# Kernel optimization log

Measured on AMD Instinct MI355X. Metric: run time of the kernel, lower is better.

## Reference

```python
import jax, jax.numpy as jnp
import numpy as np

ROPE_THETA = 10000.0


def apply_rope(q, k, cos, sin):
    # q,k: [B,H,S,D]; cos,sin: [S,D/2] -> broadcast [1,1,S,D/2]
    def rot(t):
        t2 = t.reshape(*t.shape[:-1], -1, 2)  # [B,H,S,D/2,2]
        te, to = t2[..., 0], t2[..., 1]
        c = cos[None, None, :, :]
        s = sin[None, None, :, :]
        re = te * c - to * s
        im = te * s + to * c
        return jnp.stack([re, im], axis=-1).reshape(t.shape)
    return rot(q), rot(k)


def setup_inputs() -> dict:
    key = jax.random.key(0)
    ks = jax.random.split(key, 4)
    B, S, D, H = 2, 2048, 1024, 16
    hd = D // H
    x = jax.random.normal(ks[0], (B, S, D), dtype=jnp.float32)
    # causal boolean mask (True = keep)
    mask = jnp.tril(jnp.ones((S, S), dtype=bool))[None, None]
    # rotary tables
    inv_freq = 1.0 / (ROPE_THETA ** (jnp.arange(0, hd, 2, dtype=jnp.float32) / hd))  # [hd/2]
    t = jnp.arange(S, dtype=jnp.float32)
    ang = t[:, None] * inv_freq[None, :]  # [S, hd/2]
    freqs_cos = jnp.cos(ang)
    freqs_sin = jnp.sin(ang)
    W_qkv = jax.random.normal(ks[1], (D, 3 * D), dtype=jnp.float32) * 0.02
    b_qkv = jnp.zeros((3 * D,), dtype=jnp.float32)
    W_o = jax.random.normal(ks[2], (D, D), dtype=jnp.float32) * 0.02
    b_o = jnp.zeros((D,), dtype=jnp.float32)
    return {"x": x, "mask": mask, "freqs_cos": freqs_cos, "freqs_sin": freqs_sin,
            "W_qkv": W_qkv, "b_qkv": b_qkv, "W_o": W_o, "b_o": b_o}


def reference(x, mask, freqs_cos, freqs_sin, W_qkv, b_qkv, W_o, b_o):
    B, S, D = x.shape
    H = 16
    hd = D // H
    scale = hd ** -0.5
    qkv = x @ W_qkv + b_qkv  # [B,S,3D]
    q, k, v = jnp.split(qkv, 3, axis=-1)
    q = q.reshape(B, S, H, hd).transpose(0, 2, 1, 3)  # [B,H,S,hd]
    k = k.reshape(B, S, H, hd).transpose(0, 2, 1, 3)
    v = v.reshape(B, S, H, hd).transpose(0, 2, 1, 3)
    q, k = apply_rope(q, k, freqs_cos, freqs_sin)
    scores = jnp.einsum('bhqd,bhkd->bhqk', q, k) * scale
    scores = jnp.where(mask, scores, jnp.finfo(scores.dtype).min)
    attn = jax.nn.softmax(scores, axis=-1)
    out = jnp.einsum('bhqk,bhkd->bhqd', attn, v)
    out = out.transpose(0, 2, 1, 3).reshape(B, S, D)
    return out @ W_o + b_o
```

## Files before the change

kernel.cpp:

```cpp
#include <hip/hip_runtime.h>
#include <hip/hip_bf16.h>
#include <stdint.h>

typedef unsigned short u16;
typedef __attribute__((ext_vector_type(8))) __bf16 bf16x8;
typedef __attribute__((ext_vector_type(4))) float f32x4;
typedef __attribute__((ext_vector_type(16))) float f32x16;
typedef __attribute__((ext_vector_type(8))) u16 u16x8;

__device__ __forceinline__ u16 f2bf(float f) {
  union { float f; unsigned int u; } v; v.f = f;
  unsigned int r = v.u + 0x7fffu + ((v.u >> 16) & 1u);
  return (u16)(r >> 16);
}
__device__ __forceinline__ unsigned pack2(float lo, float hi) {
  return (unsigned)f2bf(lo) | ((unsigned)f2bf(hi) << 16);
}

__device__ __forceinline__ f32x4 mfma16(bf16x8 a, bf16x8 b, f32x4 c) {
  return __builtin_amdgcn_mfma_f32_16x16x32_bf16(a, b, c, 0, 0, 0);
}
__device__ __forceinline__ f32x16 mfma32(bf16x8 a, bf16x8 b, f32x16 c) {
  return __builtin_amdgcn_mfma_f32_32x32x16_bf16(a, b, c, 0, 0, 0);
}

__device__ __forceinline__ void gload16(const void* g, void* l) {
  __builtin_amdgcn_global_load_lds((const __attribute__((address_space(1))) void*)g,
                                   (__attribute__((address_space(3))) void*)l,
                                   16, 0, 0);
}

__global__ void cast_bf16_kernel(const float* __restrict__ in, u16* __restrict__ out, int n) {
  int i = (blockIdx.x * 256 + threadIdx.x) * 8;
  if (i >= n) return;
  const float4* p = (const float4*)(in + i);
  float4 a = p[0], b = p[1];
  u16x8 o;
  o[0] = f2bf(a.x); o[1] = f2bf(a.y); o[2] = f2bf(a.z); o[3] = f2bf(a.w);
  o[4] = f2bf(b.x); o[5] = f2bf(b.y); o[6] = f2bf(b.z); o[7] = f2bf(b.w);
  *(u16x8*)(out + i) = o;
}

__global__ void transpose_cast_k(const float* __restrict__ in, u16* __restrict__ out,
                                 int R, int Ccols) {
  __shared__ float tile[64][65];
  const int c0 = (int)blockIdx.x << 6, r0 = (int)blockIdx.y << 6;
  const int tx = threadIdx.x & 63, ty = threadIdx.x >> 6;
#pragma unroll
  for (int i = ty; i < 64; i += 4)
    tile[i][tx] = in[(size_t)(r0 + i) * Ccols + c0 + tx];
  __syncthreads();
#pragma unroll
  for (int i = ty; i < 64; i += 4)
    out[(size_t)(c0 + i) * R + r0 + tx] = f2bf(tile[tx][i]);
}

__global__ __launch_bounds__(256, 2)
void gemm_bt(const u16* __restrict__ A, const u16* __restrict__ Bt,
             const float* __restrict__ bias, float* __restrict__ C,
             int M, int N, int K) {
  __shared__ u16 As[128 * 32];
  __shared__ u16 Bs[128 * 32];
  const int nb = N >> 7;
  const int m0 = (int)(blockIdx.x / nb) << 7;
  const int n0 = (int)(blockIdx.x % nb) << 7;
  const int tid = threadIdx.x;
  const int l = tid & 63, lg = l >> 4, ll = l & 15;
  const int w = tid >> 6;
  const int wr = (w >> 1) << 6, wc = (w & 1) << 6;
  const int srow = tid >> 2, scol = (tid & 3) << 3;
  const u16* ga = A + (size_t)(m0 + srow) * K + scol;
  const u16* gb = Bt + (size_t)(n0 + srow) * K + scol;
  u16* la0 = &As[srow * 32 + scol];
  u16* la1 = &As[(srow + 64) * 32 + scol];
  u16* lb0 = &Bs[srow * 32 + scol];
  u16* lb1 = &Bs[(srow + 64) * 32 + scol];
  const size_t K64 = (size_t)64 * K;
  f32x4 acc[4][4] = {};
  for (int kt = 0; kt < K; kt += 32) {
    gload16(ga + kt, la0);
    gload16(ga + kt + K64, la1);
    gload16(gb + kt, lb0);
    gload16(gb + kt + K64, lb1);
    __syncthreads();
    bf16x8 a[4], b[4];
#pragma unroll
    for (int i = 0; i < 4; ++i) {
      a[i] = *(const bf16x8*)&As[(wr + i * 16 + ll) * 32 + lg * 8];
      b[i] = *(const bf16x8*)&Bs[(wc + i * 16 + ll) * 32 + lg * 8];
    }
#pragma unroll
    for (int mi = 0; mi < 4; ++mi)
#pragma unroll
      for (int ni = 0; ni < 4; ++ni)
        acc[mi][ni] = mfma16(a[mi], b[ni], acc[mi][ni]);
    __syncthreads();
  }
#pragma unroll
  for (int mi = 0; mi < 4; ++mi) {
#pragma unroll
    for (int r = 0; r < 4; ++r) {
      const int row = m0 + wr + mi * 16 + lg * 4 + r;
      float* crow = C + (size_t)row * N + n0 + wc;
#pragma unroll
      for (int ni = 0; ni < 4; ++ni)
        crow[ni * 16 + ll] = acc[mi][ni][r] + bias[n0 + wc + ni * 16 + ll];
    }
  }
}

__global__ void rope_split_k(const float* __restrict__ qkv,
                             const float* __restrict__ fc, const float* __restrict__ fs,
                             u16* __restrict__ qr, u16* __restrict__ kr) {
  const int t = blockIdx.x;
  const int b = t >> 11, s = t & 2047;
  const int h = threadIdx.x >> 5, i = threadIdx.x & 31;
  const float c = fc[s * 32 + i], sn = fs[s * 32 + i];
  const float* qp = qkv + (size_t)t * 3072 + (h << 6) + 2 * i;
  const float qe = qp[0], qo = qp[1];
  const float ke = qp[1024], ko = qp[1025];
  const size_t ob = (((size_t)((b << 4) + h) << 11) + s) * 64 + 2 * i;
  qr[ob]     = f2bf((qe * c - qo * sn) * 0.125f);
  qr[ob + 1] = f2bf((qe * sn + qo * c) * 0.125f);
  kr[ob]     = f2bf(ke * c - ko * sn);
  kr[ob + 1] = f2bf(ke * sn + ko * c);
}

__global__ void v_transpose_k(const float* __restrict__ qkv, u16* __restrict__ vt) {
  __shared__ float tile[64][65];
  const int bh = blockIdx.x;
  const int b = bh >> 4, h = bh & 15;
  const int s0 = (int)blockIdx.y << 6;
  const int tx = threadIdx.x & 63, ty = threadIdx.x >> 6;
#pragma unroll
  for (int i = ty; i < 64; i += 4)
    tile[i][tx] = qkv[(size_t)((b << 11) + s0 + i) * 3072 + 2048 + (h << 6) + tx];
  __syncthreads();
#pragma unroll
  for (int i = ty; i < 64; i += 4)
    vt[((size_t)(bh << 6) + i) * 2048 + s0 + tx] = f2bf(tile[tx][i]);
}

__global__ __launch_bounds__(256, 2)
void attn_k(const u16* __restrict__ qr, const u16* __restrict__ kr,
            const u16* __restrict__ vt, u16* __restrict__ aout) {
  __shared__ __align__(16) char kvlds[16384];
  const int bi = (int)blockIdx.x;
  const int bh = bi & 31;
  const int qt = (bi < 256) ? (15 - (bi >> 5)) : ((bi - 256) >> 5);
  const int tid = threadIdx.x;
  const int w = tid >> 6, l = tid & 63, hi = l >> 5, ql = l & 31;
  const u16* Q  = qr + (size_t)bh * (2048 * 64);
  const u16* Kp = kr + (size_t)bh * (2048 * 64);
  const u16* Vp = vt + (size_t)bh * (64 * 2048);
  const int q0w = (qt << 7) + (w << 5);
  const int qg = q0w + ql;
  bf16x8 qf[4];
#pragma unroll
  for (int mi = 0; mi < 4; ++mi)
    qf[mi] = *(const bf16x8*)&Q[(size_t)qg * 64 + mi * 16 + hi * 8];
  const int sr = tid >> 2, sc = (tid & 3) * 32;
  const int wo0 = (sr * 128 + sc) ^ ((sr & 7) << 4);
  const int wo1 = (sr * 128 + sc + 16) ^ ((sr & 7) << 4);
  const char* kga = (const char*)(Kp + (size_t)sr * 64) + sc;
  const char* vga = (const char*)(Vp + (size_t)sr * 2048) + sc;
  const int swz = (ql & 7) << 4;
  f32x16 oa = {}, ob = {};
  float mrow = -1e30f, lp = 0.f;
  const int nch = 2 * qt + 2;
  uint4 sk0 = *(const uint4*)(kga), sk1 = *(const uint4*)(kga + 16);
  uint4 sv0 = *(const uint4*)(vga), sv1 = *(const uint4*)(vga + 16);
  for (int ch = 0; ch < nch; ++ch) {
    asm volatile("s_waitcnt vmcnt(0)" ::: "memory");
    asm volatile("s_barrier" ::: "memory");
    *(uint4*)(kvlds + wo0) = sk0;
    *(uint4*)(kvlds + wo1) = sk1;
    *(uint4*)(kvlds + 8192 + wo0) = sv0;
    *(uint4*)(kvlds + 8192 + wo1) = sv1;
    if (ch + 1 < nch) {
      const size_t kof = (size_t)(ch + 1) * 8192;
      const size_t vof = (size_t)(ch + 1) * 128;
      sk0 = *(const uint4*)(kga + kof); sk1 = *(const uint4*)(kga + kof + 16);
      sv0 = *(const uint4*)(vga + vof); sv1 = *(const uint4*)(vga + vof + 16);
    }
    asm volatile("s_waitcnt lgkmcnt(0)" ::: "memory");
    asm volatile("s_barrier" ::: "memory");
    const int kb = ch << 6;
    if (kb > q0w + 31) continue;
    f32x16 s0 = {}, s1 = {};
#pragma unroll
    for (int mi = 0; mi < 4; ++mi) {
      const int cb = mi * 32 + hi * 16;
      const bf16x8 k0 = *(const bf16x8*)(kvlds + ((ql * 128 + cb) ^ swz));
      const bf16x8 k1 = *(const bf16x8*)(kvlds + (((32 + ql) * 128 + cb) ^ swz));
      s0 = mfma32(k0, qf[mi], s0);
      s1 = mfma32(k1, qf[mi], s1);
    }
    if (kb + 63 > q0w) {
#pragma unroll
      for (int r = 0; r < 16; ++r) {
        const int kvo = (r & 3) + 8 * (r >> 2) + 4 * hi;
        if (kb + kvo > qg) s0[r] = -1e30f;
        if (kb + 32 + kvo > qg) s1[r] = -1e30f;
      }
    }
    float mx = s0[0];
#pragma unroll
    for (int r = 1; r < 16; ++r) mx = fmaxf(mx, s0[r]);
#pragma unroll
    for (int r = 0; r < 16; ++r) mx = fmaxf(mx, s1[r]);
    mx = fmaxf(mx, __shfl_xor(mx, 32));
    if (!__all(mx <= mrow + 8.f)) {
      const float mn = fmaxf(mrow, mx);
      const float esc = __expf(mrow - mn);
      mrow = mn;
      lp *= esc;
#pragma unroll
      for (int r = 0; r < 16; ++r) { oa[r] *= esc; ob[r] *= esc; }
    }
    float p0[16], p1[16];
#pragma unroll
    for (int r = 0; r < 16; ++r) {
      p0[r] = __expf(s0[r] - mrow);
      p1[r] = __expf(s1[r] - mrow);
      lp += p0[r] + p1[r];
    }
    bf16x8 pb[4];
#pragma unroll
    for (int s = 0; s < 2; ++s) {
      const float* ps = s ? p1 : p0;
#pragma unroll
      for (int j = 0; j < 2; ++j) {
        const unsigned X0 = pack2(ps[j * 8 + 0], ps[j * 8 + 1]);
        const unsigned X1 = pack2(ps[j * 8 + 2], ps[j * 8 + 3]);
        const unsigned Y0 = pack2(ps[j * 8 + 4], ps[j * 8 + 5]);
        const unsigned Y1 = pack2(ps[j * 8 + 6], ps[j * 8 + 7]);
        const unsigned sX0 = (unsigned)__shfl_xor((int)X0, 32);
        const unsigned sX1 = (unsigned)__shfl_xor((int)X1, 32);
        const unsigned sY0 = (unsigned)__shfl_xor((int)Y0, 32);
        const unsigned sY1 = (unsigned)__shfl_xor((int)Y1, 32);
        union { unsigned u[4]; bf16x8 v; } t;
        t.u[0] = hi ? sY0 : X0;
        t.u[1] = hi ? sY1 : X1;
        t.u[2] = hi ? Y0 : sX0;
        t.u[3] = hi ? Y1 : sX1;
        pb[s * 2 + j] = t.v;
      }
    }
#pragma unroll
    for (int jj = 0; jj < 4; ++jj) {
      const int cb = jj * 32 + hi * 16;
      const bf16x8 va = *(const bf16x8*)(kvlds + 8192 + ((ql * 128 + cb) ^ swz));
      const bf16x8 vb = *(const bf16x8*)(kvlds + 8192 + (((32 + ql) * 128 + cb) ^ swz));
      oa = mfma32(va, pb[jj], oa);
      ob = mfma32(vb, pb[jj], ob);
    }
  }
  lp += __shfl_xor(lp, 32);
  const float inv = 1.0f / lp;
  const int hcol = (bh & 15) << 6;
  const int tok = ((bh >> 4) << 11) + qg;
  unsigned* orow = (unsigned*)(aout + (size_t)tok * 1024 + hcol);
#pragma unroll
  for (int r = 0; r < 16; r += 2) {
    const int d0 = (r & 3) + 8 * (r >> 2) + 4 * hi;
    orow[d0 >> 1]        = pack2(oa[r] * inv, oa[r + 1] * inv);
    orow[(32 + d0) >> 1] = pack2(ob[r] * inv, ob[r + 1] * inv);
  }
}

extern "C" void kernel_launch(void* const* d_in, const int* in_sizes, int n_in,
                              void* d_out, int out_size, void* d_ws, size_t ws_size,
                              hipStream_t stream) {
  const float* x    = (const float*)d_in[0];
  const float* fc   = (const float*)d_in[2];
  const float* fs   = (const float*)d_in[3];
  const float* Wqkv = (const float*)d_in[4];
  const float* bqkv = (const float*)d_in[5];
  const float* Wo   = (const float*)d_in[6];
  const float* bo   = (const float*)d_in[7];
  float* out = (float*)d_out;

  size_t off = 0;
  auto alloc = [&](size_t bytes) {
    void* p = (char*)d_ws + off;
    off += (bytes + 255) & ~(size_t)255;
    return p;
  };
  u16*   xb   = (u16*)  alloc(4096ull * 1024 * 2);
  u16*   wqt  = (u16*)  alloc(3072ull * 1024 * 2);
  u16*   wot  = (u16*)  alloc(1024ull * 1024 * 2);
  float* qkvf = (float*)alloc(4096ull * 3072 * 4);
  u16*   qr_  = (u16*)  alloc(32ull * 2048 * 64 * 2);
  u16*   kr_  = (u16*)  alloc(32ull * 2048 * 64 * 2);
  u16*   vt_  = (u16*)  alloc(32ull * 64 * 2048 * 2);
  u16*   ao_  = (u16*)  alloc(4096ull * 1024 * 2);

  cast_bf16_kernel<<<2048, 256, 0, stream>>>(x, xb, 4096 * 1024);
  transpose_cast_k<<<dim3(48, 16), 256, 0, stream>>>(Wqkv, wqt, 1024, 3072);
  transpose_cast_k<<<dim3(16, 16), 256, 0, stream>>>(Wo, wot, 1024, 1024);
  gemm_bt<<<dim3(32 * 24), 256, 0, stream>>>(xb, wqt, bqkv, qkvf, 4096, 3072, 1024);
  rope_split_k<<<dim3(4096), 512, 0, stream>>>(qkvf, fc, fs, qr_, kr_);
  v_transpose_k<<<dim3(32, 32), 256, 0, stream>>>(qkvf, vt_);
  attn_k<<<dim3(512), 256, 0, stream>>>(qr_, kr_, vt_, ao_);
  gemm_bt<<<dim3(32 * 8), 256, 0, stream>>>(ao_, wot, bo, out, 4096, 1024, 1024);
}
```

Baseline: 143.2 us.

## Double-buffer attention K/V tiles with direct global-to-LDS loads and smaller blocks

The attention kernel now uses 128-thread blocks over 64-query tiles, launching 1024 blocks instead of 512. K/V chunks are double-buffered in LDS and filled with asynchronous global-to-LDS loads for the next chunk, replacing the register-staged copy and its extra barrier. Work on the upper half of the diagonal causal chunk is skipped, MFMA sections are wrapped in s_setprio, and the row max uses a tree reduction. The intent is to hide memory latency and cut wasted causal work, at the cost of twice the LDS per block and a trailing barrier each iteration.

```diff
diff --git a/kernel.cpp b/kernel.cpp
--- a/kernel.cpp
+++ b/kernel.cpp
@@ -141,61 +141,80 @@
     vt[((size_t)(bh << 6) + i) * 2048 + s0 + tx] = f2bf(tile[tx][i]);
 }
 
-__global__ __launch_bounds__(256, 2)
+__global__ __launch_bounds__(128, 2)
 void attn_k(const u16* __restrict__ qr, const u16* __restrict__ kr,
             const u16* __restrict__ vt, u16* __restrict__ aout) {
-  __shared__ __align__(16) char kvlds[16384];
+  __shared__ __align__(16) char kvlds[2][16384];
   const int bi = (int)blockIdx.x;
   const int bh = bi & 31;
-  const int qt = (bi < 256) ? (15 - (bi >> 5)) : ((bi - 256) >> 5);
+  const int qb = 31 - (bi >> 5);
   const int tid = threadIdx.x;
   const int w = tid >> 6, l = tid & 63, hi = l >> 5, ql = l & 31;
   const u16* Q  = qr + (size_t)bh * (2048 * 64);
   const u16* Kp = kr + (size_t)bh * (2048 * 64);
   const u16* Vp = vt + (size_t)bh * (64 * 2048);
-  const int q0w = (qt << 7) + (w << 5);
+  const int q0w = (qb << 6) + (w << 5);
   const int qg = q0w + ql;
   bf16x8 qf[4];
 #pragma unroll
   for (int mi = 0; mi < 4; ++mi)
     qf[mi] = *(const bf16x8*)&Q[(size_t)qg * 64 + mi * 16 + hi * 8];
-  const int sr = tid >> 2, sc = (tid & 3) * 32;
-  const int wo0 = (sr * 128 + sc) ^ ((sr & 7) << 4);
-  const int wo1 = (sr * 128 + sc + 16) ^ ((sr & 7) << 4);
-  const char* kga = (const char*)(Kp + (size_t)sr * 64) + sc;
-  const char* vga = (const char*)(Vp + (size_t)sr * 2048) + sc;
+  const int grow = l >> 3;
+  const int gcol = (((l & 7) ^ grow) << 4);
+  const char* kbase = (const char*)Kp + (size_t)(w * 32 + grow) * 128 + gcol;
+  const char* vbase = (const char*)Vp + (size_t)(w * 32 + grow) * 4096 + gcol;
+  char* const lk = (char*)kvlds + (w << 12) + l * 16;
+  char* const lv = (char*)kvlds + 8192 + (w << 12) + l * 16;
   const int swz = (ql & 7) << 4;
   f32x16 oa = {}, ob = {};
   float mrow = -1e30f, lp = 0.f;
-  const int nch = 2 * qt + 2;
-  uint4 sk0 = *(const uint4*)(kga), sk1 = *(const uint4*)(kga + 16);
-  uint4 sv0 = *(const uint4*)(vga), sv1 = *(const uint4*)(vga + 16);
+  const int nch = qb + 1;
+  {
+    const char* kg = kbase; const char* vg = vbase;
+#pragma unroll
+    for (int c = 0; c < 4; ++c) {
+      gload16(kg + c * 1024, lk + c * 1024);
+      gload16(vg + c * 32768, lv + c * 1024);
+    }
+  }
+  int cur = 0;
   for (int ch = 0; ch < nch; ++ch) {
-    asm volatile("s_waitcnt vmcnt(0)" ::: "memory");
+    if (ch + 1 < nch) {
+      const char* kg = kbase + (size_t)(ch + 1) * 8192;
+      const char* vg = vbase + (size_t)(ch + 1) * 128;
+      char* nk = lk + ((cur ^ 1) << 14);
+      char* nv = lv + ((cur ^ 1) << 14);
+#pragma unroll
+      for (int c = 0; c < 4; ++c) {
+        gload16(kg + c * 1024, nk + c * 1024);
+        gload16(vg + c * 32768, nv + c * 1024);
+      }
+      asm volatile("s_waitcnt vmcnt(8)" ::: "memory");
+    } else {
+      asm volatile("s_waitcnt vmcnt(0)" ::: "memory");
+    }
     asm volatile("s_barrier" ::: "memory");
-    *(uint4*)(kvlds + wo0) = sk0;
-    *(uint4*)(kvlds + wo1) = sk1;
-    *(uint4*)(kvlds + 8192 + wo0) = sv0;
-    *(uint4*)(kvlds + 8192 + wo1) = sv1;
-    if (ch + 1 < nch) {
-      const size_t kof = (size_t)(ch + 1) * 8192;
-      const size_t vof = (size_t)(ch + 1) * 128;
-      sk0 = *(const uint4*)(kga + kof); sk1 = *(const uint4*)(kga + kof + 16);
-      sv0 = *(const uint4*)(vga + vof); sv1 = *(const uint4*)(vga + vof + 16);
-    }
-    asm volatile("s_waitcnt lgkmcnt(0)" ::: "memory");
-    asm volatile("s_barrier" ::: "memory");
+    const char* kbuf = (const char*)kvlds + (cur << 14);
+    const char* vbuf = kbuf + 8192;
     const int kb = ch << 6;
-    if (kb > q0w + 31) continue;
+    const bool dohi = (kb + 32) <= (q0w + 31);
     f32x16 s0 = {}, s1 = {};
+    __builtin_amdgcn_s_setprio(1);
 #pragma unroll
     for (int mi = 0; mi < 4; ++mi) {
       const int cb = mi * 32 + hi * 16;
-      const bf16x8 k0 = *(const bf16x8*)(kvlds + ((ql * 128 + cb) ^ swz));
-      const bf16x8 k1 = *(const bf16x8*)(kvlds + (((32 + ql) * 128 + cb) ^ swz));
+      const bf16x8 k0 = *(const bf16x8*)(kbuf + ((ql * 128 + cb) ^ swz));
       s0 = mfma32(k0, qf[mi], s0);
-      s1 = mfma32(k1, qf[mi], s1);
-    }
+    }
+    if (dohi) {
+#pragma unroll
+      for (int mi = 0; mi < 4; ++mi) {
+        const int cb = mi * 32 + hi * 16;
+        const bf16x8 k1 = *(const bf16x8*)(kbuf + (((32 + ql) * 128 + cb) ^ swz));
+        s1 = mfma32(k1, qf[mi], s1);
+      }
+    }
+    __builtin_amdgcn_s_setprio(0);
     if (kb + 63 > q0w) {
 #pragma unroll
       for (int r = 0; r < 16; ++r) {
@@ -204,12 +223,20 @@
         if (kb + 32 + kvo > qg) s1[r] = -1e30f;
       }
     }
-    float mx = s0[0];
-#pragma unroll
-    for (int r = 1; r < 16; ++r) mx = fmaxf(mx, s0[r]);
-#pragma unroll
-    for (int r = 0; r < 16; ++r) mx = fmaxf(mx, s1[r]);
-    mx = fmaxf(mx, __shfl_xor(mx, 32));
+    float a[16];
+    if (dohi) {
+#pragma unroll
+      for (int r = 0; r < 16; ++r) a[r] = fmaxf(s0[r], s1[r]);
+    } else {
+#pragma unroll
+      for (int r = 0; r < 16; ++r) a[r] = s0[r];
+    }
+#pragma unroll
+    for (int st = 8; st > 0; st >>= 1)
+#pragma unroll
+      for (int j = 0; j < 8; ++j)
+        if (j < st) a[j] = fmaxf(a[j], a[j + st]);
+    float mx = fmaxf(a[0], __shfl_xor(a[0], 32));
     if (!__all(mx <= mrow + 8.f)) {
       const float mn = fmaxf(mrow, mx);
       const float esc = __expf(mrow - mn);
@@ -222,12 +249,20 @@
 #pragma unroll
     for (int r = 0; r < 16; ++r) {
       p0[r] = __expf(s0[r] - mrow);
-      p1[r] = __expf(s1[r] - mrow);
-      lp += p0[r] + p1[r];
+      lp += p0[r];
+    }
+    if (dohi) {
+#pragma unroll
+      for (int r = 0; r < 16; ++r) {
+        p1[r] = __expf(s1[r] - mrow);
+        lp += p1[r];
+      }
     }
     bf16x8 pb[4];
+    const int nseg = dohi ? 2 : 1;
 #pragma unroll
     for (int s = 0; s < 2; ++s) {
+      if (s >= nseg) break;
       const float* ps = s ? p1 : p0;
 #pragma unroll
       for (int j = 0; j < 2; ++j) {
@@ -247,14 +282,20 @@
         pb[s * 2 + j] = t.v;
       }
     }
+    const int njj = dohi ? 4 : 2;
+    __builtin_amdgcn_s_setprio(1);
 #pragma unroll
     for (int jj = 0; jj < 4; ++jj) {
+      if (jj >= njj) break;
       const int cb = jj * 32 + hi * 16;
-      const bf16x8 va = *(const bf16x8*)(kvlds + 8192 + ((ql * 128 + cb) ^ swz));
-      const bf16x8 vb = *(const bf16x8*)(kvlds + 8192 + (((32 + ql) * 128 + cb) ^ swz));
+      const bf16x8 va = *(const bf16x8*)(vbuf + ((ql * 128 + cb) ^ swz));
+      const bf16x8 vb = *(const bf16x8*)(vbuf + (((32 + ql) * 128 + cb) ^ swz));
       oa = mfma32(va, pb[jj], oa);
       ob = mfma32(vb, pb[jj], ob);
     }
+    __builtin_amdgcn_s_setprio(0);
+    asm volatile("s_barrier" ::: "memory");
+    cur ^= 1;
   }
   lp += __shfl_xor(lp, 32);
   const float inv = 1.0f / lp;
@@ -302,6 +343,6 @@
   gemm_bt<<<dim3(32 * 24), 256, 0, stream>>>(xb, wqt, bqkv, qkvf, 4096, 3072, 1024);
   rope_split_k<<<dim3(4096), 512, 0, stream>>>(qkvf, fc, fs, qr_, kr_);
   v_transpose_k<<<dim3(32, 32), 256, 0, stream>>>(qkvf, vt_);
-  attn_k<<<dim3(512), 256, 0, stream>>>(qr_, kr_, vt_, ao_);
+  attn_k<<<dim3(1024), 128, 0, stream>>>(qr_, kr_, vt_, ao_);
   gemm_bt<<<dim3(32 * 8), 256, 0, stream>>>(ao_, wot, bo, out, 4096, 1024, 1024);
 }
```

Result: slower. 155.6 us (+8.7%).

## Fuse RoPE, scaling and head split into QKV GEMM epilogue

Applied to the files above, without the earlier changes.

Adds a specialised QKV GEMM whose epilogue applies the bias, rotary embedding (using a lane shuffle to fetch the paired element) and the Q scaling, then writes bf16 Q/K/V directly in per-head layout. This removes the fp32 QKV intermediate buffer and the separate rope kernel. V transposition now reads bf16 instead of fp32. The epilogue does scattered 2-byte stores and per-element table loads, which may be less efficient than the old coalesced writes.

```diff
diff --git a/kernel.cpp b/kernel.cpp
--- a/kernel.cpp
+++ b/kernel.cpp
@@ -53,6 +53,76 @@
 #pragma unroll
   for (int i = ty; i < 64; i += 4)
     out[(size_t)(c0 + i) * R + r0 + tx] = f2bf(tile[tx][i]);
+}
+
+__global__ __launch_bounds__(256, 2)
+void gemm_qkv(const u16* __restrict__ A, const u16* __restrict__ Bt,
+              const float* __restrict__ bias,
+              const float* __restrict__ fc, const float* __restrict__ fs,
+              u16* __restrict__ qr, u16* __restrict__ kr, u16* __restrict__ vr) {
+  const int K = 1024;
+  __shared__ u16 As[128 * 32];
+  __shared__ u16 Bs[128 * 32];
+  const int m0 = (int)(blockIdx.x / 24) << 7;
+  const int n0 = (int)(blockIdx.x % 24) << 7;
+  const int tid = threadIdx.x;
+  const int l = tid & 63, lg = l >> 4, ll = l & 15;
+  const int w = tid >> 6;
+  const int wr = (w >> 1) << 6, wc = (w & 1) << 6;
+  const int srow = tid >> 2, scol = (tid & 3) << 3;
+  const u16* ga = A + (size_t)(m0 + srow) * K + scol;
+  const u16* gb = Bt + (size_t)(n0 + srow) * K + scol;
+  u16* la0 = &As[srow * 32 + scol];
+  u16* la1 = &As[(srow + 64) * 32 + scol];
+  u16* lb0 = &Bs[srow * 32 + scol];
+  u16* lb1 = &Bs[(srow + 64) * 32 + scol];
+  const size_t K64 = (size_t)64 * K;
+  f32x4 acc[4][4] = {};
+  for (int kt = 0; kt < K; kt += 32) {
+    gload16(ga + kt, la0);
+    gload16(ga + kt + K64, la1);
+    gload16(gb + kt, lb0);
+    gload16(gb + kt + K64, lb1);
+    __syncthreads();
+    bf16x8 a[4], b[4];
+#pragma unroll
+    for (int i = 0; i < 4; ++i) {
+      a[i] = *(const bf16x8*)&As[(wr + i * 16 + ll) * 32 + lg * 8];
+      b[i] = *(const bf16x8*)&Bs[(wc + i * 16 + ll) * 32 + lg * 8];
+    }
+#pragma unroll
+    for (int mi = 0; mi < 4; ++mi)
+#pragma unroll
+      for (int ni = 0; ni < 4; ++ni)
+        acc[mi][ni] = mfma16(a[mi], b[ni], acc[mi][ni]);
+    __syncthreads();
+  }
+  const int sec = n0 >> 10;
+  u16* const dst = (sec == 0) ? qr : (sec == 1) ? kr : vr;
+#pragma unroll
+  for (int ni = 0; ni < 4; ++ni) {
+    const int n = n0 + wc + ni * 16 + ll;
+    const int h = (n & 1023) >> 6, d = n & 63;
+    const float bi_ = bias[n];
+    const int i2 = d >> 1;
+    const bool odd = d & 1;
+#pragma unroll
+    for (int mi = 0; mi < 4; ++mi) {
+#pragma unroll
+      for (int r = 0; r < 4; ++r) {
+        const int row = m0 + wr + mi * 16 + lg * 4 + r;
+        const int b = row >> 11, s = row & 2047;
+        float v = acc[mi][ni][r] + bi_;
+        if (sec < 2) {
+          const float c = fc[s * 32 + i2], sn = fs[s * 32 + i2];
+          const float p = __shfl_xor(v, 1);
+          v = odd ? (p * sn + v * c) : (v * c - p * sn);
+          if (sec == 0) v *= 0.125f;
+        }
+        dst[((size_t)(((b << 4) + h) << 11 | s)) * 64 + d] = f2bf(v);
+      }
+    }
+  }
 }
 
 __global__ __launch_bounds__(256, 2)
@@ -109,36 +179,18 @@
   }
 }
 
-__global__ void rope_split_k(const float* __restrict__ qkv,
-                             const float* __restrict__ fc, const float* __restrict__ fs,
-                             u16* __restrict__ qr, u16* __restrict__ kr) {
-  const int t = blockIdx.x;
-  const int b = t >> 11, s = t & 2047;
-  const int h = threadIdx.x >> 5, i = threadIdx.x & 31;
-  const float c = fc[s * 32 + i], sn = fs[s * 32 + i];
-  const float* qp = qkv + (size_t)t * 3072 + (h << 6) + 2 * i;
-  const float qe = qp[0], qo = qp[1];
-  const float ke = qp[1024], ko = qp[1025];
-  const size_t ob = (((size_t)((b << 4) + h) << 11) + s) * 64 + 2 * i;
-  qr[ob]     = f2bf((qe * c - qo * sn) * 0.125f);
-  qr[ob + 1] = f2bf((qe * sn + qo * c) * 0.125f);
-  kr[ob]     = f2bf(ke * c - ko * sn);
-  kr[ob + 1] = f2bf(ke * sn + ko * c);
-}
-
-__global__ void v_transpose_k(const float* __restrict__ qkv, u16* __restrict__ vt) {
-  __shared__ float tile[64][65];
+__global__ void v_transpose_bf16(const u16* __restrict__ vr, u16* __restrict__ vt) {
+  __shared__ u16 tile[64][66];
   const int bh = blockIdx.x;
-  const int b = bh >> 4, h = bh & 15;
   const int s0 = (int)blockIdx.y << 6;
   const int tx = threadIdx.x & 63, ty = threadIdx.x >> 6;
 #pragma unroll
   for (int i = ty; i < 64; i += 4)
-    tile[i][tx] = qkv[(size_t)((b << 11) + s0 + i) * 3072 + 2048 + (h << 6) + tx];
+    tile[i][tx] = vr[((size_t)bh * 2048 + s0 + i) * 64 + tx];
   __syncthreads();
 #pragma unroll
   for (int i = ty; i < 64; i += 4)
-    vt[((size_t)(bh << 6) + i) * 2048 + s0 + tx] = f2bf(tile[tx][i]);
+    vt[((size_t)bh * 64 + i) * 2048 + s0 + tx] = tile[tx][i];
 }
 
 __global__ __launch_bounds__(256, 2)
@@ -290,18 +342,17 @@
   u16*   xb   = (u16*)  alloc(4096ull * 1024 * 2);
   u16*   wqt  = (u16*)  alloc(3072ull * 1024 * 2);
   u16*   wot  = (u16*)  alloc(1024ull * 1024 * 2);
-  float* qkvf = (float*)alloc(4096ull * 3072 * 4);
   u16*   qr_  = (u16*)  alloc(32ull * 2048 * 64 * 2);
   u16*   kr_  = (u16*)  alloc(32ull * 2048 * 64 * 2);
+  u16*   vr_  = (u16*)  alloc(32ull * 2048 * 64 * 2);
   u16*   vt_  = (u16*)  alloc(32ull * 64 * 2048 * 2);
   u16*   ao_  = (u16*)  alloc(4096ull * 1024 * 2);
 
   cast_bf16_kernel<<<2048, 256, 0, stream>>>(x, xb, 4096 * 1024);
   transpose_cast_k<<<dim3(48, 16), 256, 0, stream>>>(Wqkv, wqt, 1024, 3072);
   transpose_cast_k<<<dim3(16, 16), 256, 0, stream>>>(Wo, wot, 1024, 1024);
-  gemm_bt<<<dim3(32 * 24), 256, 0, stream>>>(xb, wqt, bqkv, qkvf, 4096, 3072, 1024);
-  rope_split_k<<<dim3(4096), 512, 0, stream>>>(qkvf, fc, fs, qr_, kr_);
-  v_transpose_k<<<dim3(32, 32), 256, 0, stream>>>(qkvf, vt_);
+  gemm_qkv<<<dim3(32 * 24), 256, 0, stream>>>(xb, wqt, bqkv, fc, fs, qr_, kr_, vr_);
+  v_transpose_bf16<<<dim3(32, 32), 256, 0, stream>>>(vr_, vt_);
   attn_k<<<dim3(512), 256, 0, stream>>>(qr_, kr_, vt_, ao_);
   gemm_bt<<<dim3(32 * 8), 256, 0, stream>>>(ao_, wot, bo, out, 4096, 1024, 1024);
 }
```

Measured after the change: 141.4 us. About the same (-1.3%).
